# Kernel optimization log

Measured on AMD Instinct MI355X. Metric: run time of the kernel, lower is better.

The kernel has to match this reference:

```python
import jax, jax.numpy as jnp
import numpy as np

N_HITS = 49152
HIT_F = 256
INST_F = 32
N_IT_CONST = 1024
Q_MIN = 0.5   # ObjCondensationLoss default q_min
S_B = 1.0     # ObjCondensationLoss default background strength


def setup_inputs() -> dict:
    key = jax.random.key(0)
    ks = jax.random.split(key, 6)
    x = jax.random.normal(ks[0], (N_HITS, HIT_F), jnp.float32)
    W_beta = jax.random.normal(ks[1], (HIT_F, 1), jnp.float32) / np.sqrt(HIT_F).astype(np.float32)
    b_beta = jnp.zeros((1,), jnp.float32)
    W_coord = jax.random.normal(ks[2], (HIT_F, INST_F), jnp.float32) / np.sqrt(HIT_F).astype(np.float32)
    b_coord = jnp.zeros((INST_F,), jnp.float32)
    temp = jnp.zeros((), jnp.float32)  # nn.Parameter(torch.tensor(0.0))
    # true instance labels per hit; pin first N_IT hits so every instance is populated
    y_i = jax.random.randint(ks[3], (N_HITS,), 0, N_IT_CONST)
    y_i = y_i.at[:N_IT_CONST].set(jnp.arange(N_IT_CONST))
    idx = jnp.arange(N_HITS)
    noise = (idx % 5 == 0) & (idx >= N_IT_CONST)
    y_i = jnp.where(noise, -1, y_i).astype(jnp.int64)
    y_semantic = jax.random.randint(ks[4], (N_HITS,), 0, 7).astype(jnp.int32)
    # hit -> true-instance membership edges (E_H_IT), fixed shape built eagerly
    yv = np.asarray(y_i)
    e0 = np.nonzero(yv >= 0)[0]
    edge_index = jnp.asarray(np.stack([e0, yv[e0]]), dtype=jnp.int32)
    return {"x": x, "W_beta": W_beta, "b_beta": b_beta, "W_coord": W_coord,
            "b_coord": b_coord, "temp": temp, "y_i": y_i,
            "y_semantic": y_semantic, "edge_index": edge_index, "n_it": N_IT_CONST}


def _obj_condensation_loss(ox, beta, y_i, edge_index, n_it):
    """Object condensation loss -> stack([background_loss, potential_loss])."""
    n = ox.shape[0]
    beta_c = jnp.clip(beta, 1e-4, 1.0 - 1e-4)
    q = jnp.arctanh(beta_c) ** 2 + Q_MIN  # charge per hit, [N]
    e_h, e_i = edge_index[0], edge_index[1]
    qe = q[e_h]
    # condensation point alpha_k = member hit with max charge (segment argmax)
    seg_max = jax.ops.segment_max(qe, e_i, num_segments=n_it)
    is_max = qe >= seg_max[e_i]
    alpha = jax.ops.segment_min(jnp.where(is_max, e_h, n), e_i, num_segments=n_it)
    alpha = jnp.clip(alpha, 0, n - 1)
    x_a = ox[alpha]        # [K, D]
    q_a = q[alpha]         # [K]
    beta_a = beta_c[alpha]  # [K]
    # attractive potential over membership edges: q_i * q_alpha * ||x_i - x_alpha||^2
    d2_att = jnp.sum((ox[e_h] - x_a[e_i]) ** 2, axis=-1)
    v_att = jnp.sum(qe * q_a[e_i] * d2_att)
    # repulsive potential over all (hit, instance) non-member pairs: hinge(1 - dist)
    d2 = (jnp.sum(ox * ox, axis=1)[:, None] + jnp.sum(x_a * x_a, axis=1)[None, :]
          - 2.0 * ox @ x_a.T)  # [N, K]
    dist = jnp.sqrt(jnp.maximum(d2, 0.0) + 1e-12)
    hinge = jnp.maximum(1.0 - dist, 0.0)
    member = jnp.zeros((n, n_it), jnp.float32).at[e_h, e_i].set(1.0)
    v_rep = jnp.sum((q[:, None] * q_a[None, :]) * hinge * (1.0 - member))
    l_v = (v_att + v_rep) / n
    # background loss: push beta_alpha -> 1, noise-hit beta -> 0
    noise = y_i < 0
    n_noise = jnp.maximum(jnp.sum(noise), 1)
    l_b = jnp.mean(1.0 - beta_a) + S_B * jnp.sum(jnp.where(noise, beta_c, 0.0)) / n_noise
    return jnp.stack([l_b, l_v])


def reference(x, W_beta, b_beta, W_coord, b_coord, temp, y_i, y_semantic, edge_index, n_it):
    beta = jax.nn.sigmoid(x @ W_beta + b_beta)[:, 0]  # h.of, [N]
    ox = x @ W_coord + b_coord                        # h.ox, [N, D]
    loss_vec = _obj_condensation_loss(ox, beta, y_i, edge_index, n_it)
    loss_vec = loss_vec * jnp.exp(-temp)  # temperature-weighted (b, v)
    return loss_vec.sum() + temp          # train-stage scalar loss
```

## Files before the change

### kernel.cpp

```cpp
#include <hip/hip_runtime.h>
#include <math.h>

#define NH 49152
#define KI 1024
#define DD 32
#define HF 256
#define REPB 768

#define WS_PART  0
#define WS_SEG64 8
#define WS_WT    2056
#define WS_A12   (WS_WT + 8448)
#define WS_H12   (WS_A12 + 12*KI)
#define WS_XA    (WS_H12 + 12*NH)
#define WS_OX    (WS_XA + KI*DD)

typedef __attribute__((address_space(1))) const unsigned int gu32;
typedef __attribute__((address_space(3))) unsigned int lu32;

__device__ __forceinline__ float rl(float v, int lane) {
    return __uint_as_float(__builtin_amdgcn_readlane(__float_as_uint(v), lane));
}

__global__ __launch_bounds__(256) void k_prep(const float* __restrict__ Wc,
                                              const float* __restrict__ Wb,
                                              float* __restrict__ ws) {
    const int i = blockIdx.x * 256 + threadIdx.x;
    if (i < 8192) {
        const int w = i >> 11, r2 = i & 2047;
        const int l = r2 >> 5, q = r2 & 31;
        const int dk = q >> 3, col = q & 7;
        const int k = (l >> 3) * 32 + (l & 7) * 4 + dk;
        ws[WS_WT + i] = Wc[(size_t)k * 32 + w * 8 + col];
    } else if (i < 8448) {
        const int r2 = i - 8192;
        const int l = r2 >> 2, dk = r2 & 3;
        const int k = (l >> 3) * 32 + (l & 7) * 4 + dk;
        ws[WS_WT + i] = Wb[k];
    }
    if (i < 512) *(float4*)(ws + WS_SEG64 + (size_t)i * 4) = make_float4(0.f, 0.f, 0.f, 0.f);
    if (i < 8) ws[WS_PART + i] = 0.0f;
}

__global__ __launch_bounds__(256, 3) void k_gemm(
        const float* __restrict__ x, const float* __restrict__ bb,
        const float* __restrict__ bcrd, const int* __restrict__ yi,
        float* __restrict__ ws) {
    __shared__ float xs[2][8][256];
    const int t0 = threadIdx.x;
    const int w  = __builtin_amdgcn_readfirstlane(t0 >> 6);
    const int l  = t0 & 63;
    const int h  = blockIdx.x * 64 + l;
    const float* __restrict__ wbase = ws + WS_WT + w * 2048;
    const float* __restrict__ xrow  = x + (size_t)h * HF;

    float wr[32];
    #pragma unroll
    for (int q = 0; q < 8; ++q) {
        const float4 v = *(const float4*)(wbase + l * 32 + q * 4);
        wr[q * 4 + 0] = v.x; wr[q * 4 + 1] = v.y;
        wr[q * 4 + 2] = v.z; wr[q * 4 + 3] = v.w;
    }
    float br[4] = {0.f, 0.f, 0.f, 0.f};
    if (w == 3) {
        const float4 v = *(const float4*)(ws + WS_WT + 8192 + l * 4);
        br[0] = v.x; br[1] = v.y; br[2] = v.z; br[3] = v.w;
    }

    float acc[8];
    #pragma unroll
    for (int j = 0; j < 8; ++j) acc[j] = 0.0f;
    float accb = 0.0f;

#define STAGE(buf, c1) { \
    const float* s0 = xrow + (c1) * 32 + (2 * w) * 4; \
    __builtin_amdgcn_global_load_lds((gu32*)(const void*)s0, \
        (lu32*)(void*)&xs[buf][2 * w][0], 16, 0, 0); \
    const float* s1 = s0 + 4; \
    __builtin_amdgcn_global_load_lds((gu32*)(const void*)s1, \
        (lu32*)(void*)&xs[buf][2 * w + 1][0], 16, 0, 0); }

#define DK(dk, xc) { \
    acc[0] = fmaf(xc, rl(wr[(dk)*8 + 0], ls), acc[0]); \
    acc[1] = fmaf(xc, rl(wr[(dk)*8 + 1], ls), acc[1]); \
    acc[2] = fmaf(xc, rl(wr[(dk)*8 + 2], ls), acc[2]); \
    acc[3] = fmaf(xc, rl(wr[(dk)*8 + 3], ls), acc[3]); \
    acc[4] = fmaf(xc, rl(wr[(dk)*8 + 4], ls), acc[4]); \
    acc[5] = fmaf(xc, rl(wr[(dk)*8 + 5], ls), acc[5]); \
    acc[6] = fmaf(xc, rl(wr[(dk)*8 + 6], ls), acc[6]); \
    acc[7] = fmaf(xc, rl(wr[(dk)*8 + 7], ls), acc[7]); \
    if (w == 3) accb = fmaf(xc, rl(br[dk], ls), accb); }

    STAGE(0, 0);
    __syncthreads();
    for (int c = 0; c < 8; ++c) {
        if (c < 7) STAGE((c + 1) & 1, c + 1);
        const int lb = c * 8;
        #pragma unroll
        for (int t = 0; t < 8; ++t) {
            const float4 xv = *(const float4*)&xs[c & 1][t][l * 4];
            const int ls = lb + t;
            DK(0, xv.x)
            DK(1, xv.y)
            DK(2, xv.z)
            DK(3, xv.w)
        }
        __syncthreads();
    }

    const float4 ba0 = *(const float4*)(bcrd + w * 8);
    const float4 ba1 = *(const float4*)(bcrd + w * 8 + 4);
    const float4 o0 = {acc[0] + ba0.x, acc[1] + ba0.y, acc[2] + ba0.z, acc[3] + ba0.w};
    const float4 o1 = {acc[4] + ba1.x, acc[5] + ba1.y, acc[6] + ba1.z, acc[7] + ba1.w};
    *(float4*)(ws + WS_OX + (size_t)h * DD + w * 8)     = o0;
    *(float4*)(ws + WS_OX + (size_t)h * DD + w * 8 + 4) = o1;

    if (w == 0) {
        const float s8 = o0.x*o0.x + o0.y*o0.y + o0.z*o0.z + o0.w*o0.w
                       + o1.x*o1.x + o1.y*o1.y + o1.z*o1.z + o1.w*o1.w;
        float* hr = ws + WS_H12 + (size_t)h * 12;
        *(float4*)(hr)     = o0;
        *(float4*)(hr + 4) = o1;
        hr[8] = 0.5f * s8;
    }
    if (w == 3) {
        const float z    = accb + bb[0];
        const float beta = 1.0f / (1.0f + expf(-z));
        const float bcv  = fminf(fmaxf(beta, 1e-4f), 0.9999f);
        const float at   = atanhf(bcv);
        float* hr = ws + WS_H12 + (size_t)h * 12;
        hr[9]  = at * at + 0.5f;
        hr[10] = bcv;
        const int y = yi[h];
        float    nb  = (y < 0) ? bcv : 0.0f;
        unsigned cnt = (y < 0) ? 1u : 0u;
        for (int off = 32; off > 0; off >>= 1) {
            nb  += __shfl_down(nb, off);
            cnt += __shfl_down(cnt, off);
        }
        if (l == 0) {
            atomicAdd(ws + WS_PART + 2, nb);
            atomicAdd((unsigned int*)(ws + WS_PART + 3), cnt);
        }
    }
}

__global__ __launch_bounds__(256) void k_segmax(const int* __restrict__ eh, const int* __restrict__ ei,
                                                int E, const float* __restrict__ h12,
                                                unsigned long long* __restrict__ seg) {
    int e = blockIdx.x * 256 + threadIdx.x;
    if (e < E) {
        int h = eh[e];
        float q = h12[(size_t)h * 12 + 9];
        unsigned long long pk = ((unsigned long long)__float_as_uint(q) << 32)
                              | (unsigned)(NH - 1 - h);
        atomicMax(seg + ei[e], pk);
    }
}

__global__ __launch_bounds__(256) void k_gather(float* __restrict__ ws) {
    const int k = blockIdx.x * 256 + threadIdx.x;
    unsigned long long pk = ((const unsigned long long*)(ws + WS_SEG64))[k];
    int a = NH - 1 - (int)(unsigned)(pk & 0xffffffffu);
    a = max(0, min(a, NH - 1));
    float4 v0, v1;
    float s8 = 0.0f;
    #pragma unroll
    for (int d0 = 0; d0 < DD; d0 += 4) {
        float4 v = *(const float4*)(ws + WS_OX + (size_t)a * DD + d0);
        *(float4*)(ws + WS_XA + (size_t)k * DD + d0) = v;
        if (d0 == 0) { v0 = v; s8 += v.x*v.x + v.y*v.y + v.z*v.z + v.w*v.w; }
        if (d0 == 4) { v1 = v; s8 += v.x*v.x + v.y*v.y + v.z*v.z + v.w*v.w; }
    }
    *(float4*)(ws + WS_A12 + (size_t)k * 12)     = v0;
    *(float4*)(ws + WS_A12 + (size_t)k * 12 + 4) = v1;
    ws[WS_A12 + (size_t)k * 12 + 8] = 0.5f * (s8 - 1.0f);
    ws[WS_A12 + (size_t)k * 12 + 9] = ws[WS_H12 + (size_t)a * 12 + 9];
    float omba = 1.0f - ws[WS_H12 + (size_t)a * 12 + 10];
    for (int off = 32; off > 0; off >>= 1) omba += __shfl_down(omba, off);
    if ((threadIdx.x & 63) == 0) atomicAdd(ws + WS_PART + 4, omba);
}

__global__ __launch_bounds__(256, 4) void k_attrep(
        const int* __restrict__ eh, const int* __restrict__ ei, int E,
        const int* __restrict__ yi, float* __restrict__ ws) {
    __shared__ float al[128 * 12];
    __shared__ float red[4];
    const float* __restrict__ a12 = ws + WS_A12;
    const float* __restrict__ h12 = ws + WS_H12;
    const float* __restrict__ ox  = ws + WS_OX;
    const float* __restrict__ xa  = ws + WS_XA;
    const int t = threadIdx.x;

    if (blockIdx.x >= REPB) {
        const int e = (blockIdx.x - REPB) * 256 + t;
        float cv = 0.0f;
        if (e < E) {
            const int h = eh[e], k = ei[e];
            const float* a = ox + (size_t)h * DD;
            const float* b = xa + (size_t)k * DD;
            float d2 = 0.0f;
            #pragma unroll
            for (int d0 = 0; d0 < DD; d0 += 4) {
                float4 av = *(const float4*)(a + d0);
                float4 bv = *(const float4*)(b + d0);
                float dx = av.x - bv.x; d2 = fmaf(dx, dx, d2);
                float dy = av.y - bv.y; d2 = fmaf(dy, dy, d2);
                float dz = av.z - bv.z; d2 = fmaf(dz, dz, d2);
                float dw = av.w - bv.w; d2 = fmaf(dw, dw, d2);
            }
            cv = h12[(size_t)h * 12 + 9] * a12[(size_t)k * 12 + 9] * d2;
        }
        for (int off = 32; off > 0; off >>= 1) cv += __shfl_down(cv, off);
        if ((t & 63) == 0) red[t >> 6] = cv;
        __syncthreads();
        if (t == 0) atomicAdd(ws + WS_PART + 1, red[0] + red[1] + red[2] + red[3]);
        return;
    }

    const int bh = blockIdx.x % 96;
    const int bk = blockIdx.x / 96;
    const int k0 = bk * 128;
    for (int i = t; i < 128 * 12; i += 256)
        al[i] = a12[(size_t)k0 * 12 + i];
    __syncthreads();

    const int h1 = bh * 512 + t;
    const int h2 = h1 + 256;
    const float4 p0  = *(const float4*)(h12 + (size_t)h1 * 12);
    const float4 p1  = *(const float4*)(h12 + (size_t)h1 * 12 + 4);
    const float2 cq1 = *(const float2*)(h12 + (size_t)h1 * 12 + 8);
    const float4 s0  = *(const float4*)(h12 + (size_t)h2 * 12);
    const float4 s1  = *(const float4*)(h12 + (size_t)h2 * 12 + 4);
    const float2 cq2 = *(const float2*)(h12 + (size_t)h2 * 12 + 8);
    const int yh1 = yi[h1], yh2 = yi[h2];
    float loc = 0.0f;

    #pragma unroll 4
    for (int r = 0; r < 128; ++r) {
        const float4 b0  = *(const float4*)(al + r * 12);
        const float4 b1  = *(const float4*)(al + r * 12 + 4);
        const float2 bcq = *(const float2*)(al + r * 12 + 8);
        float acc1 = -cq1.x - bcq.x;
        acc1 = fmaf(p0.x, b0.x, acc1);
        acc1 = fmaf(p0.y, b0.y, acc1);
        acc1 = fmaf(p0.z, b0.z, acc1);
        acc1 = fmaf(p0.w, b0.w, acc1);
        acc1 = fmaf(p1.x, b1.x, acc1);
        acc1 = fmaf(p1.y, b1.y, acc1);
        acc1 = fmaf(p1.z, b1.z, acc1);
        acc1 = fmaf(p1.w, b1.w, acc1);
        float acc2 = -cq2.x - bcq.x;
        acc2 = fmaf(s0.x, b0.x, acc2);
        acc2 = fmaf(s0.y, b0.y, acc2);
        acc2 = fmaf(s0.z, b0.z, acc2);
        acc2 = fmaf(s0.w, b0.w, acc2);
        acc2 = fmaf(s1.x, b1.x, acc2);
        acc2 = fmaf(s1.y, b1.y, acc2);
        acc2 = fmaf(s1.z, b1.z, acc2);
        acc2 = fmaf(s1.w, b1.w, acc2);
        if (acc1 > 0.0f) {
            const int kg = k0 + r;
            if (yh1 != kg) {
                float d2 = 1.0f - 2.0f * acc1;
                const float* hp  = ox + (size_t)h1 * DD;
                const float* apf = xa + (size_t)kg * DD;
                #pragma unroll
                for (int d = 8; d < DD; d += 4) {
                    float4 av = *(const float4*)(hp + d);
                    float4 bv = *(const float4*)(apf + d);
                    float dx = av.x - bv.x; d2 = fmaf(dx, dx, d2);
                    float dy = av.y - bv.y; d2 = fmaf(dy, dy, d2);
                    float dz = av.z - bv.z; d2 = fmaf(dz, dz, d2);
                    float dw = av.w - bv.w; d2 = fmaf(dw, dw, d2);
                }
                float dist = sqrtf(fmaxf(d2, 0.0f) + 1e-12f);
                float hin  = 1.0f - dist;
                if (hin > 0.0f) loc += cq1.y * bcq.y * hin;
            }
        }
        if (acc2 > 0.0f) {
            const int kg = k0 + r;
            if (yh2 != kg) {
                float d2 = 1.0f - 2.0f * acc2;
                const float* hp  = ox + (size_t)h2 * DD;
                const float* apf = xa + (size_t)kg * DD;
                #pragma unroll
                for (int d = 8; d < DD; d += 4) {
                    float4 av = *(const float4*)(hp + d);
                    float4 bv = *(const float4*)(apf + d);
                    float dx = av.x - bv.x; d2 = fmaf(dx, dx, d2);
                    float dy = av.y - bv.y; d2 = fmaf(dy, dy, d2);
                    float dz = av.z - bv.z; d2 = fmaf(dz, dz, d2);
                    float dw = av.w - bv.w; d2 = fmaf(dw, dw, d2);
                }
                float dist = sqrtf(fmaxf(d2, 0.0f) + 1e-12f);
                float hin  = 1.0f - dist;
                if (hin > 0.0f) loc += cq2.y * bcq.y * hin;
            }
        }
    }
    for (int off = 32; off > 0; off >>= 1) loc += __shfl_down(loc, off);
    if ((t & 63) == 0) red[t >> 6] = loc;
    __syncthreads();
    if (t == 0) atomicAdd(ws + WS_PART + 0, red[0] + red[1] + red[2] + red[3]);
}

__global__ void k_final(const float* __restrict__ temp, float* __restrict__ ws,
                        float* __restrict__ out) {
    float vrep  = ws[WS_PART + 0];
    float vatt  = ws[WS_PART + 1];
    float nsum  = ws[WS_PART + 2];
    unsigned nn = *(const unsigned int*)(ws + WS_PART + 3);
    float somba = ws[WS_PART + 4];
    float lb = somba * (1.0f / (float)KI) + nsum / (float)(nn < 1u ? 1u : nn);
    float lv = (vatt + vrep) / (float)NH;
    float tv = temp[0];
    out[0] = (lb + lv) * expf(-tv) + tv;
}

extern "C" void kernel_launch(void* const* d_in, const int* in_sizes, int n_in,
                              void* d_out, int out_size, void* d_ws, size_t ws_size,
                              hipStream_t stream) {
    const float* x    = (const float*)d_in[0];
    const float* Wb   = (const float*)d_in[1];
    const float* bb   = (const float*)d_in[2];
    const float* Wc   = (const float*)d_in[3];
    const float* bcrd = (const float*)d_in[4];
    const float* temp = (const float*)d_in[5];
    const int*   yi   = (const int*)d_in[6];
    const int*   ep   = (const int*)d_in[8];
    const int E = in_sizes[8] / 2;
    const int* eh = ep;
    const int* ei = ep + E;
    float* ws  = (float*)d_ws;
    float* out = (float*)d_out;

    k_prep<<<33, 256, 0, stream>>>(Wc, Wb, ws);
    k_gemm<<<NH / 64, 256, 0, stream>>>(x, bb, bcrd, yi, ws);
    const int eb = (E + 255) / 256;
    k_segmax<<<eb, 256, 0, stream>>>(eh, ei, E, ws + WS_H12,
                                     (unsigned long long*)(ws + WS_SEG64));
    k_gather<<<KI / 256, 256, 0, stream>>>(ws);
    k_attrep<<<REPB + eb, 256, 0, stream>>>(eh, ei, E, yi, ws);
    k_final<<<1, 1, 0, stream>>>(temp, ws, out);
}
```

Measured before the change: 117.3 us.

## Compute hit projection GEMM with split-bf16 MFMA instead of scalar FMA

Replaces the scalar-FMA readlane GEMM for x@W_coord and x@W_beta with 16x16x32 bf16 MFMA instructions, using a three-term hi/lo bf16 split to keep close to fp32 accuracy. Weights are pre-split into hi and lo bf16 tiles in the prep kernel, and x is loaded straight into registers without the LDS staging. The goal is to cut the ALU-bound FMA cost of the projection. In exchange it adds per-element conversion work and a small precision loss from dropping the lo*lo term.

```diff
diff --git a/kernel.cpp b/kernel.cpp
--- a/kernel.cpp
+++ b/kernel.cpp
@@ -7,36 +7,45 @@
 #define HF 256
 #define REPB 768
 
+typedef __attribute__((ext_vector_type(8))) short bf16x8;
+typedef __attribute__((ext_vector_type(4))) float f32x4;
+
 #define WS_PART  0
 #define WS_SEG64 8
-#define WS_WT    2056
-#define WS_A12   (WS_WT + 8448)
+#define WS_BH    2056
+#define WS_BL    (WS_BH + 6144)
+#define WS_A12   (WS_BL + 6144)
 #define WS_H12   (WS_A12 + 12*KI)
 #define WS_XA    (WS_H12 + 12*NH)
 #define WS_OX    (WS_XA + KI*DD)
 
-typedef __attribute__((address_space(1))) const unsigned int gu32;
-typedef __attribute__((address_space(3))) unsigned int lu32;
-
-__device__ __forceinline__ float rl(float v, int lane) {
-    return __uint_as_float(__builtin_amdgcn_readlane(__float_as_uint(v), lane));
+__device__ __forceinline__ unsigned short bf16rne(float f) {
+    unsigned u = __float_as_uint(f);
+    unsigned r = u + 0x7FFFu + ((u >> 16) & 1u);
+    return (unsigned short)(r >> 16);
 }
 
 __global__ __launch_bounds__(256) void k_prep(const float* __restrict__ Wc,
                                               const float* __restrict__ Wb,
                                               float* __restrict__ ws) {
     const int i = blockIdx.x * 256 + threadIdx.x;
-    if (i < 8192) {
-        const int w = i >> 11, r2 = i & 2047;
-        const int l = r2 >> 5, q = r2 & 31;
-        const int dk = q >> 3, col = q & 7;
-        const int k = (l >> 3) * 32 + (l & 7) * 4 + dk;
-        ws[WS_WT + i] = Wc[(size_t)k * 32 + w * 8 + col];
-    } else if (i < 8448) {
-        const int r2 = i - 8192;
-        const int l = r2 >> 2, dk = r2 & 3;
-        const int k = (l >> 3) * 32 + (l & 7) * 4 + dk;
-        ws[WS_WT + i] = Wb[k];
+    if (i < 12288) {
+        const int tile = i >> 12;
+        const int r2 = i & 4095;
+        const int kw = r2 >> 9;
+        const int lr = r2 & 511;
+        const int l = lr >> 3, r = lr & 7;
+        const int k = kw * 32 + (l >> 4) * 8 + r;
+        const int n = l & 15;
+        float v;
+        if (tile == 0)      v = Wc[(size_t)k * 32 + n];
+        else if (tile == 1) v = Wc[(size_t)k * 32 + 16 + n];
+        else                v = (n == 0) ? Wb[k] : 0.0f;
+        const unsigned short hi = bf16rne(v);
+        const float hf = __uint_as_float((unsigned)hi << 16);
+        const unsigned short lo = bf16rne(v - hf);
+        ((unsigned short*)(ws + WS_BH))[i] = hi;
+        ((unsigned short*)(ws + WS_BL))[i] = lo;
     }
     if (i < 512) *(float4*)(ws + WS_SEG64 + (size_t)i * 4) = make_float4(0.f, 0.f, 0.f, 0.f);
     if (i < 8) ws[WS_PART + i] = 0.0f;
@@ -46,102 +55,97 @@
         const float* __restrict__ x, const float* __restrict__ bb,
         const float* __restrict__ bcrd, const int* __restrict__ yi,
         float* __restrict__ ws) {
-    __shared__ float xs[2][8][256];
-    const int t0 = threadIdx.x;
-    const int w  = __builtin_amdgcn_readfirstlane(t0 >> 6);
-    const int l  = t0 & 63;
-    const int h  = blockIdx.x * 64 + l;
-    const float* __restrict__ wbase = ws + WS_WT + w * 2048;
-    const float* __restrict__ xrow  = x + (size_t)h * HF;
-
-    float wr[32];
+    const int t = threadIdx.x;
+    const int w = t >> 6;
+    const int l = t & 63;
+    const int col = l & 15;
+    const int kg  = l >> 4;
+    const int h0 = blockIdx.x * 64 + w * 16;
+    const unsigned short* __restrict__ bhp = (const unsigned short*)(ws + WS_BH);
+    const unsigned short* __restrict__ blp = (const unsigned short*)(ws + WS_BL);
+    const float* __restrict__ xp = x + (size_t)(h0 + col) * HF + kg * 8;
+
+    float4 xv[8][2];
     #pragma unroll
-    for (int q = 0; q < 8; ++q) {
-        const float4 v = *(const float4*)(wbase + l * 32 + q * 4);
-        wr[q * 4 + 0] = v.x; wr[q * 4 + 1] = v.y;
-        wr[q * 4 + 2] = v.z; wr[q * 4 + 3] = v.w;
-    }
-    float br[4] = {0.f, 0.f, 0.f, 0.f};
-    if (w == 3) {
-        const float4 v = *(const float4*)(ws + WS_WT + 8192 + l * 4);
-        br[0] = v.x; br[1] = v.y; br[2] = v.z; br[3] = v.w;
-    }
-
-    float acc[8];
+    for (int kw = 0; kw < 8; ++kw) {
+        xv[kw][0] = *(const float4*)(xp + kw * 32);
+        xv[kw][1] = *(const float4*)(xp + kw * 32 + 4);
+    }
+
+    f32x4 a0 = {0.f, 0.f, 0.f, 0.f};
+    f32x4 a1 = {0.f, 0.f, 0.f, 0.f};
+    f32x4 a2 = {0.f, 0.f, 0.f, 0.f};
+
     #pragma unroll
-    for (int j = 0; j < 8; ++j) acc[j] = 0.0f;
-    float accb = 0.0f;
-
-#define STAGE(buf, c1) { \
-    const float* s0 = xrow + (c1) * 32 + (2 * w) * 4; \
-    __builtin_amdgcn_global_load_lds((gu32*)(const void*)s0, \
-        (lu32*)(void*)&xs[buf][2 * w][0], 16, 0, 0); \
-    const float* s1 = s0 + 4; \
-    __builtin_amdgcn_global_load_lds((gu32*)(const void*)s1, \
-        (lu32*)(void*)&xs[buf][2 * w + 1][0], 16, 0, 0); }
-
-#define DK(dk, xc) { \
-    acc[0] = fmaf(xc, rl(wr[(dk)*8 + 0], ls), acc[0]); \
-    acc[1] = fmaf(xc, rl(wr[(dk)*8 + 1], ls), acc[1]); \
-    acc[2] = fmaf(xc, rl(wr[(dk)*8 + 2], ls), acc[2]); \
-    acc[3] = fmaf(xc, rl(wr[(dk)*8 + 3], ls), acc[3]); \
-    acc[4] = fmaf(xc, rl(wr[(dk)*8 + 4], ls), acc[4]); \
-    acc[5] = fmaf(xc, rl(wr[(dk)*8 + 5], ls), acc[5]); \
-    acc[6] = fmaf(xc, rl(wr[(dk)*8 + 6], ls), acc[6]); \
-    acc[7] = fmaf(xc, rl(wr[(dk)*8 + 7], ls), acc[7]); \
-    if (w == 3) accb = fmaf(xc, rl(br[dk], ls), accb); }
-
-    STAGE(0, 0);
-    __syncthreads();
-    for (int c = 0; c < 8; ++c) {
-        if (c < 7) STAGE((c + 1) & 1, c + 1);
-        const int lb = c * 8;
+    for (int kw = 0; kw < 8; ++kw) {
+        const int base = (kw * 64 + l) * 8;
+        const bf16x8 B0h = *(const bf16x8*)(bhp + base);
+        const bf16x8 B0l = *(const bf16x8*)(blp + base);
+        const bf16x8 B1h = *(const bf16x8*)(bhp + 4096 + base);
+        const bf16x8 B1l = *(const bf16x8*)(blp + 4096 + base);
+        const bf16x8 B2h = *(const bf16x8*)(bhp + 8192 + base);
+        const bf16x8 B2l = *(const bf16x8*)(blp + 8192 + base);
+
+        bf16x8 Ah, Al;
+        const float* xf = (const float*)&xv[kw][0];
         #pragma unroll
-        for (int t = 0; t < 8; ++t) {
-            const float4 xv = *(const float4*)&xs[c & 1][t][l * 4];
-            const int ls = lb + t;
-            DK(0, xv.x)
-            DK(1, xv.y)
-            DK(2, xv.z)
-            DK(3, xv.w)
-        }
-        __syncthreads();
-    }
-
-    const float4 ba0 = *(const float4*)(bcrd + w * 8);
-    const float4 ba1 = *(const float4*)(bcrd + w * 8 + 4);
-    const float4 o0 = {acc[0] + ba0.x, acc[1] + ba0.y, acc[2] + ba0.z, acc[3] + ba0.w};
-    const float4 o1 = {acc[4] + ba1.x, acc[5] + ba1.y, acc[6] + ba1.z, acc[7] + ba1.w};
-    *(float4*)(ws + WS_OX + (size_t)h * DD + w * 8)     = o0;
-    *(float4*)(ws + WS_OX + (size_t)h * DD + w * 8 + 4) = o1;
-
-    if (w == 0) {
-        const float s8 = o0.x*o0.x + o0.y*o0.y + o0.z*o0.z + o0.w*o0.w
-                       + o1.x*o1.x + o1.y*o1.y + o1.z*o1.z + o1.w*o1.w;
-        float* hr = ws + WS_H12 + (size_t)h * 12;
-        *(float4*)(hr)     = o0;
-        *(float4*)(hr + 4) = o1;
-        hr[8] = 0.5f * s8;
-    }
-    if (w == 3) {
-        const float z    = accb + bb[0];
-        const float beta = 1.0f / (1.0f + expf(-z));
-        const float bcv  = fminf(fmaxf(beta, 1e-4f), 0.9999f);
-        const float at   = atanhf(bcv);
-        float* hr = ws + WS_H12 + (size_t)h * 12;
-        hr[9]  = at * at + 0.5f;
-        hr[10] = bcv;
-        const int y = yi[h];
-        float    nb  = (y < 0) ? bcv : 0.0f;
-        unsigned cnt = (y < 0) ? 1u : 0u;
-        for (int off = 32; off > 0; off >>= 1) {
-            nb  += __shfl_down(nb, off);
-            cnt += __shfl_down(cnt, off);
-        }
-        if (l == 0) {
-            atomicAdd(ws + WS_PART + 2, nb);
-            atomicAdd((unsigned int*)(ws + WS_PART + 3), cnt);
-        }
+        for (int r = 0; r < 8; ++r) {
+            const float v = xf[r];
+            const unsigned short hi = bf16rne(v);
+            const float hf = __uint_as_float((unsigned)hi << 16);
+            const unsigned short lo = bf16rne(v - hf);
+            Ah[r] = (short)hi;
+            Al[r] = (short)lo;
+        }
+        a0 = __builtin_amdgcn_mfma_f32_16x16x32_bf16(Ah, B0h, a0, 0, 0, 0);
+        a1 = __builtin_amdgcn_mfma_f32_16x16x32_bf16(Ah, B1h, a1, 0, 0, 0);
+        a2 = __builtin_amdgcn_mfma_f32_16x16x32_bf16(Ah, B2h, a2, 0, 0, 0);
+        a0 = __builtin_amdgcn_mfma_f32_16x16x32_bf16(Ah, B0l, a0, 0, 0, 0);
+        a1 = __builtin_amdgcn_mfma_f32_16x16x32_bf16(Ah, B1l, a1, 0, 0, 0);
+        a2 = __builtin_amdgcn_mfma_f32_16x16x32_bf16(Ah, B2l, a2, 0, 0, 0);
+        a0 = __builtin_amdgcn_mfma_f32_16x16x32_bf16(Al, B0h, a0, 0, 0, 0);
+        a1 = __builtin_amdgcn_mfma_f32_16x16x32_bf16(Al, B1h, a1, 0, 0, 0);
+        a2 = __builtin_amdgcn_mfma_f32_16x16x32_bf16(Al, B2h, a2, 0, 0, 0);
+    }
+
+    const float bc0 = bcrd[col];
+    const float bc1 = bcrd[16 + col];
+    const float bb0 = bb[0];
+    float nb = 0.0f;
+    unsigned cnt = 0u;
+    #pragma unroll
+    for (int r = 0; r < 4; ++r) {
+        const int h = h0 + kg * 4 + r;
+        const float o0 = a0[r] + bc0;
+        const float o1 = a1[r] + bc1;
+        ws[WS_OX + (size_t)h * DD + col]      = o0;
+        ws[WS_OX + (size_t)h * DD + 16 + col] = o1;
+        float sq = (col < 8) ? o0 * o0 : 0.0f;
+        sq += __shfl_xor(sq, 1);
+        sq += __shfl_xor(sq, 2);
+        sq += __shfl_xor(sq, 4);
+        sq += __shfl_xor(sq, 8);
+        if (col < 8) ws[WS_H12 + (size_t)h * 12 + col] = o0;
+        if (col == 0) {
+            float* hr = ws + WS_H12 + (size_t)h * 12;
+            hr[8] = 0.5f * sq;
+            const float z    = a2[r] + bb0;
+            const float beta = 1.0f / (1.0f + expf(-z));
+            const float bcv  = fminf(fmaxf(beta, 1e-4f), 0.9999f);
+            const float at   = atanhf(bcv);
+            hr[9]  = at * at + 0.5f;
+            hr[10] = bcv;
+            const int y = yi[h];
+            if (y < 0) { nb += bcv; cnt += 1u; }
+        }
+    }
+    for (int off = 32; off > 0; off >>= 1) {
+        nb  += __shfl_down(nb, off);
+        cnt += __shfl_down(cnt, off);
+    }
+    if (l == 0) {
+        atomicAdd(ws + WS_PART + 2, nb);
+        atomicAdd((unsigned int*)(ws + WS_PART + 3), cnt);
     }
 }
 
@@ -336,7 +340,7 @@
     float* ws  = (float*)d_ws;
     float* out = (float*)d_out;
 
-    k_prep<<<33, 256, 0, stream>>>(Wc, Wb, ws);
+    k_prep<<<48, 256, 0, stream>>>(Wc, Wb, ws);
     k_gemm<<<NH / 64, 256, 0, stream>>>(x, bb, bcrd, yi, ws);
     const int eb = (E + 255) / 256;
     k_segmax<<<eb, 256, 0, stream>>>(eh, ei, E, ws + WS_H12,
```

After: 141.2 us. +20.3%, slower.
